# Optimization experiments

Hardware: AMD Instinct MI355X
Metric: run time of the kernel (lower is better)

Reference implementation:

```python
import jax, jax.numpy as jnp
import numpy as np

# dims
B, N, D = 256, 77, 768     # batch, CLIP tokens, token dim
K, Dn, H = 16, 768, 8      # nodes, node dim, heads
HID, L = 512, 2            # edge-MLP hidden, num GNN layers


def setup_inputs() -> dict:
    key = jax.random.key(0)
    ks = jax.random.split(key, 12)
    g = lambda k, shape, s=0.02: (jax.random.normal(k, shape, jnp.float32) * s)
    return {
        "w": jax.random.normal(ks[0], (B, N, D), jnp.float32),
        "token_mask": jax.random.randint(ks[1], (B, N), 0, 2).astype(jnp.int32),
        "node_queries": g(ks[2], (1, K, Dn)),
        "Wq": g(ks[3], (Dn, Dn)), "bq": jnp.zeros((Dn,), jnp.float32),
        "Wk": g(ks[4], (D, Dn)),  "bk": jnp.zeros((Dn,), jnp.float32),
        "Wv": g(ks[5], (D, Dn)),  "bv": jnp.zeros((Dn,), jnp.float32),
        "We1": g(ks[6], (2 * Dn, HID)), "be1": jnp.zeros((HID,), jnp.float32),
        "We2": g(ks[7], (HID, 1)),      "be2": jnp.zeros((1,), jnp.float32),
        "fuse_gate": jnp.float32(0.0),
        "Wg": g(ks[8], (L, Dn, Dn)), "bg": jnp.zeros((L, Dn), jnp.float32),
    }


def _edge_logits(V, We1, be1, We2, be2):
    # edge_mlp(cat[Vi, Vj]) without materializing [B,K,K,2Dn]:
    # split first linear into the Vi-half and Vj-half of its weight.
    hi = V @ We1[:Dn]   # [B,K,HID]
    hj = V @ We1[Dn:]   # [B,K,HID]
    h = jax.nn.relu(hi[:, :, None, :] + hj[:, None, :, :] + be1)  # [B,K,K,HID]
    return jnp.einsum('bijh,h->bij', h, We2[:, 0]) + be2[0]       # [B,K,K]


def _forward(w, node_queries, Wq, bq, Wk, bk, Wv, bv,
             We1, be1, We2, be2, fuse_gate, Wg, bg, token_mask):
    q = jnp.broadcast_to(node_queries, (B, K, Dn))
    Q = q @ Wq + bq        # [B,K,Dn]
    Kt = w @ Wk + bk       # [B,N,Dn]
    Vt = w @ Wv + bv       # [B,N,Dn]
    # per-head dot products summed over heads == full Dn dot product
    scale = (Dn // H) ** -0.5
    scores = jnp.einsum('bkd,bnd->bkn', Q, Kt) * scale  # [B,K,N]
    pad = (token_mask == 0)[:, None, :]                 # [B,1,N]
    scores = jnp.where(pad, jnp.finfo(scores.dtype).min, scores)
    # softmax over K per token (transpose to [B,N,K])
    S = jax.nn.softmax(jnp.swapaxes(scores, 1, 2), axis=-1)  # [B,N,K]
    V = jnp.einsum('bnk,bnd->bkd', S, Vt)                    # [B,K,Dn]
    gate = jax.nn.sigmoid(fuse_gate)
    V = (1.0 - gate) * V + gate * q
    # pre-GNN edge logits, then relational GNN refinement
    E = _edge_logits(V, We1, be1, We2, be2)
    A = jax.nn.softmax(E, axis=-1)  # [B,K,K], fixed across layers
    for l in range(L):
        msg = jnp.einsum('bij,bjd->bid', A, V @ Wg[l] + bg[l])
        V = V + jax.nn.relu(msg)
    # post-GNN edge logits
    E = _edge_logits(V, We1, be1, We2, be2)
    return S, V, E


def reference(w, token_mask, node_queries, Wq, bq, Wk, bk, Wv, bv,
              We1, be1, We2, be2, fuse_gate, Wg, bg):
    return _forward(w, node_queries, Wq, bq, Wk, bk, Wv, bv,
                    We1, be1, We2, be2, fuse_gate, Wg, bg, token_mask)
```

## Files before the change

kernel.cpp:

```cpp
#include <hip/hip_runtime.h>

typedef unsigned short u16;
typedef __attribute__((ext_vector_type(8))) short short8;
typedef __attribute__((ext_vector_type(4))) float f32x4;

#define DEV static __device__ __forceinline__

DEV float bf2f(u16 u) { return __uint_as_float(((unsigned)u) << 16); }
DEV u16 f2bf(float f) {
  unsigned u = __float_as_uint(f);
  return (u16)((u + 0x7fffu + ((u >> 16) & 1u)) >> 16);
}

DEV void cp16(void* lds, const void* g) {
  __builtin_amdgcn_global_load_lds(
      (const __attribute__((address_space(1))) unsigned int*)g,
      (__attribute__((address_space(3))) unsigned int*)lds, 16, 0, 0);
}

DEV void vm_drain() { asm volatile("s_waitcnt vmcnt(0)" ::: "memory"); }


__global__ __launch_bounds__(256) void tcast_all(const float* __restrict__ Wv,
                                                 const float* __restrict__ We1,
                                                 const float* __restrict__ Wg,
                                                 u16* __restrict__ WvT,
                                                 u16* __restrict__ We1T,
                                                 u16* __restrict__ WgT) {
  __shared__ float tile[32][33];
  const float* src; u16* dst; int C;
  switch (blockIdx.z) {
    case 0: src = Wv;           dst = WvT;           C = 768; break;
    case 1: src = We1;          dst = We1T;          C = 512; break;
    case 2: src = We1 + 393216; dst = We1T + 393216; C = 512; break;
    case 3: src = Wg;           dst = WgT;           C = 768; break;
    default: src = Wg + 589824; dst = WgT + 589824;  C = 768; break;
  }
  int r0 = blockIdx.y * 32, c0 = blockIdx.x * 32;
  if (c0 >= C) return;
  int tr = threadIdx.x >> 5, tc = threadIdx.x & 31;
#pragma unroll
  for (int rr = 0; rr < 4; ++rr)
    tile[tr + rr * 8][tc] = src[(size_t)(r0 + tr + rr * 8) * C + c0 + tc];
  __syncthreads();
#pragma unroll
  for (int rr = 0; rr < 4; ++rr)
    dst[(size_t)(c0 + tr + rr * 8) * 768 + r0 + tc] = f2bf(tile[tc][tr + rr * 8]);
}

__global__ __launch_bounds__(256) void q_part(const float* __restrict__ nq,
                                              const float* __restrict__ Wq,
                                              float* __restrict__ Qpart) {
  int gid = blockIdx.x * 256 + threadIdx.x;
  int s = blockIdx.y;
  int k = gid / 768, d = gid % 768;
  const float* nr = nq + k * 768 + s * 96;
  const float* wp = Wq + (size_t)(s * 96) * 768 + d;
  float s0 = 0.f, s1 = 0.f, s2 = 0.f, s3 = 0.f;
#pragma unroll
  for (int c = 0; c < 96; c += 4) {
    s0 += nr[c + 0] * wp[(size_t)(c + 0) * 768];
    s1 += nr[c + 1] * wp[(size_t)(c + 1) * 768];
    s2 += nr[c + 2] * wp[(size_t)(c + 2) * 768];
    s3 += nr[c + 3] * wp[(size_t)(c + 3) * 768];
  }
  Qpart[(size_t)s * 12288 + gid] = (s0 + s1) + (s2 + s3);
}

__global__ __launch_bounds__(256) void q_reduce(const float* __restrict__ Qpart,
                                                const float* __restrict__ bq,
                                                float* __restrict__ Qf) {
  int gid = blockIdx.x * 256 + threadIdx.x;
  int d = gid % 768;
  float s = bq[d];
#pragma unroll
  for (int i = 0; i < 8; ++i) s += Qpart[(size_t)i * 12288 + gid];
  Qf[gid] = s;
}

__global__ __launch_bounds__(256) void pt_kernel(const float* __restrict__ Qf,
                                                 const float* __restrict__ Wk,
                                                 const float* __restrict__ bk,
                                                 u16* __restrict__ PT16,
                                                 float* __restrict__ qb) {
  int t = threadIdx.x;
  if (blockIdx.x == 48) {
    int k = t >> 4, j = t & 15;
    const float* q = Qf + k * 768 + j * 48;
    const float* bp = bk + j * 48;
    float s = 0.f;
#pragma unroll
    for (int d = 0; d < 48; d += 4) {
      f32x4 qv = *(const f32x4*)&q[d];
      f32x4 bv4 = *(const f32x4*)&bp[d];
      s += qv[0] * bv4[0] + qv[1] * bv4[1] + qv[2] * bv4[2] + qv[3] * bv4[3];
    }
#pragma unroll
    for (int off = 1; off < 16; off <<= 1) s += __shfl_xor(s, off);
    if (j == 0) qb[k] = s;
    return;
  }
  int gid = blockIdx.x * 256 + t;
  int c = gid >> 4, k = gid & 15;
  const float* wr = Wk + (size_t)c * 768;
  const float* q = Qf + k * 768;
  float s = 0.f;
  for (int d = 0; d < 768; d += 4) {
    f32x4 wv = *(const f32x4*)&wr[d];
    f32x4 qv = *(const f32x4*)&q[d];
    s += wv[0] * qv[0] + wv[1] * qv[1] + wv[2] * qv[2] + wv[3] * qv[3];
  }
  PT16[k * 768 + c] = f2bf(s);
}

__global__ __launch_bounds__(256) void score2(const float* __restrict__ w,
                                              const u16* __restrict__ PT16,
                                              const float* __restrict__ qb,
                                              const int* __restrict__ mask,
                                              float* __restrict__ Sout) {
  __shared__ u16 Ps[16 * 776];
  int t = threadIdx.x, wave = t >> 6, lane = t & 63, l16 = lane & 15, quad = lane >> 4;
  int m0 = blockIdx.x * 64;
#pragma unroll
  for (int r = 0; r < 6; ++r) {
    int idx = t + 256 * r;
    int row = idx / 96, c8 = idx % 96;
    *(short8*)&Ps[row * 776 + c8 * 8] = *(const short8*)&PT16[row * 768 + c8 * 8];
  }
  __syncthreads();
  int row = m0 + wave * 16 + l16;
  const float* ap = w + (size_t)row * 768 + quad * 8;
  f32x4 acc = {0.f, 0.f, 0.f, 0.f};
#pragma unroll
  for (int it = 0; it < 24; ++it) {
    f32x4 a0 = *(const f32x4*)(ap + it * 32);
    f32x4 a1 = *(const f32x4*)(ap + it * 32 + 4);
    short8 fa;
#pragma unroll
    for (int e = 0; e < 4; ++e) { fa[e] = (short)f2bf(a0[e]); fa[e + 4] = (short)f2bf(a1[e]); }
    short8 fb = *(const short8*)&Ps[l16 * 776 + it * 32 + quad * 8];
    acc = __builtin_amdgcn_mfma_f32_16x16x32_bf16(fa, fb, acc, 0, 0, 0);
  }
  float qv = qb[l16];
  const float scale = 0.1020620726159658f;
#pragma unroll
  for (int r = 0; r < 4; ++r) {
    int orow = m0 + wave * 16 + quad * 4 + r;
    float s = (acc[r] + qv) * scale;
    if (mask[orow] == 0) s = -3.402823466e38f;
    float mx = s;
#pragma unroll
    for (int off = 1; off < 16; off <<= 1) mx = fmaxf(mx, __shfl_xor(mx, off));
    float e = __expf(s - mx);
    float sm = e;
#pragma unroll
    for (int off = 1; off < 16; off <<= 1) sm += __shfl_xor(sm, off);
    Sout[(size_t)orow * 16 + l16] = e / sm;
  }
}

__global__ __launch_bounds__(256) void u_kernel(const float* __restrict__ Sg,
                                                const float* __restrict__ w,
                                                u16* __restrict__ U16,
                                                float* __restrict__ sk) {
  __shared__ float Ss[1232];
  int b = blockIdx.x, t = threadIdx.x;
  int d = blockIdx.y * 256 + t;
#pragma unroll
  for (int r = 0; r < 5; ++r) {
    int idx = t + 256 * r;
    if (idx < 1232) Ss[idx] = Sg[(size_t)b * 1232 + idx];
  }
  __syncthreads();
  float a[16];
#pragma unroll
  for (int k = 0; k < 16; ++k) a[k] = 0.f;
  const float* wp = w + (size_t)b * 59136;
  for (int n = 0; n < 77; ++n) {
    float g = wp[(size_t)n * 768 + d];
    const float* sr = &Ss[n * 16];
#pragma unroll
    for (int k = 0; k < 16; ++k) a[k] += sr[k] * g;
  }
#pragma unroll
  for (int k = 0; k < 16; ++k)
    U16[(size_t)b * 12288 + (size_t)k * 768 + d] = f2bf(a[k]);
  if (blockIdx.y == 0 && t < 16) {
    float s = 0.f;
    for (int n = 0; n < 77; ++n) s += Ss[n * 16 + t];
    sk[b * 16 + t] = s;
  }
}

__global__ __launch_bounds__(256) void vgemm(const u16* __restrict__ A,
                                             const u16* __restrict__ BT,
                                             const float* __restrict__ skp,
                                             const float* __restrict__ bv,
                                             const float* __restrict__ nq,
                                             const float* __restrict__ gatep,
                                             float* __restrict__ V32,
                                             u16* __restrict__ V16) {
  __shared__ u16 As[2 * 64 * 32];
  __shared__ u16 Bs[2 * 128 * 32];
  int mi = blockIdx.x / 6, ni = blockIdx.x % 6;
  int m0 = mi * 64, n0 = ni * 128;
  int t = threadIdx.x;
  int wave = t >> 6, lane = t & 63, l16 = lane & 15, quad = lane >> 4;
  int ra = wave * 16 + (lane >> 2);
  int rb1 = wave * 32 + (lane >> 2);
  int rb2 = rb1 + 16;
  int cslot = lane & 3;
  int cga = (cslot ^ ((ra >> 1) & 3)) * 8;
  int cgb1 = (cslot ^ ((rb1 >> 1) & 3)) * 8;
  int cgb2 = (cslot ^ ((rb2 >> 1) & 3)) * 8;

  const u16* Ap = A + (size_t)(m0 + ra) * 768 + cga;
  const u16* Bp1 = BT + (size_t)(n0 + rb1) * 768 + cgb1;
  const u16* Bp2 = BT + (size_t)(n0 + rb2) * 768 + cgb2;
  u16* AsW = &As[(wave * 16) * 32];
  u16* BsW1 = &Bs[(wave * 32) * 32];
  u16* BsW2 = &Bs[(wave * 32 + 16) * 32];

  f32x4 zero4 = {0.f, 0.f, 0.f, 0.f};
  f32x4 acc[4][2];
#pragma unroll
  for (int i = 0; i < 4; ++i) { acc[i][0] = zero4; acc[i][1] = zero4; }

  cp16(AsW, Ap); cp16(BsW1, Bp1); cp16(BsW2, Bp2);
  vm_drain();
  __builtin_amdgcn_s_barrier();

  int cur = 0;
  for (int k0 = 0; k0 < 768; k0 += 32) {
    int nxt = cur ^ 1;
    if (k0 + 32 < 768) {
      cp16(AsW + nxt * 2048, Ap + k0 + 32);
      cp16(BsW1 + nxt * 4096, Bp1 + k0 + 32);
      cp16(BsW2 + nxt * 4096, Bp2 + k0 + 32);
    }
    const u16* Ab = &As[cur * 2048];
    const u16* Bb = &Bs[cur * 4096];
    short8 fa[4], fb[2];
#pragma unroll
    for (int i = 0; i < 4; ++i) {
      int R = i * 16 + l16;
      fa[i] = *(const short8*)&Ab[R * 32 + (quad ^ ((R >> 1) & 3)) * 8];
    }
#pragma unroll
    for (int j = 0; j < 2; ++j) {
      int R = wave * 32 + j * 16 + l16;
      fb[j] = *(const short8*)&Bb[R * 32 + (quad ^ ((R >> 1) & 3)) * 8];
    }
#pragma unroll
    for (int i = 0; i < 4; ++i)
#pragma unroll
      for (int j = 0; j < 2; ++j)
        acc[i][j] = __builtin_amdgcn_mfma_f32_16x16x32_bf16(fa[i], fb[j], acc[i][j], 0, 0, 0);
    vm_drain();
    __builtin_amdgcn_s_barrier();
    cur = nxt;
  }

  float gv = gatep[0];
  float g = 1.f / (1.f + __expf(-gv)), og = 1.f - g;
  int narr[2]; float bvj[2];
#pragma unroll
  for (int j = 0; j < 2; ++j) {
    narr[j] = n0 + wave * 32 + j * 16 + l16;
    bvj[j] = bv[narr[j]];
  }
#pragma unroll
  for (int i = 0; i < 4; ++i)
#pragma unroll
    for (int r = 0; r < 4; ++r) {
      int m = m0 + i * 16 + quad * 4 + r;
      float skv = skp[m];
      size_t mrow = (size_t)m * 768;
      const float* nqr = nq + (m & 15) * 768;
#pragma unroll
      for (int j = 0; j < 2; ++j) {
        float val = acc[i][j][r] + skv * bvj[j];
        float v = og * val + g * nqr[narr[j]];
        V32[mrow + narr[j]] = v;
        V16[mrow + narr[j]] = f2bf(v);
      }
    }
}

__global__ __launch_bounds__(256) void gemm16s(const u16* __restrict__ A,
                                               const u16* __restrict__ BT0,
                                               const float* __restrict__ bias0,
                                               u16* __restrict__ C0, int N0, int ntA,
                                               const u16* __restrict__ BT1,
                                               const float* __restrict__ bias1,
                                               u16* __restrict__ C1, int N1, int ntB,
                                               int K) {
  __shared__ u16 As[2 * 64 * 32];
  __shared__ u16 Bs[2 * 128 * 32];
  int nt = ntA + ntB;
  int mi = blockIdx.x / nt, ni = blockIdx.x % nt;
  const u16* BT; const float* bias; u16* C; int N, n0;
  if (ni < ntA) { BT = BT0; bias = bias0; C = C0; N = N0; n0 = ni * 128; }
  else          { BT = BT1; bias = bias1; C = C1; N = N1; n0 = (ni - ntA) * 128; }
  int m0 = mi * 64;
  int t = threadIdx.x;
  int wave = t >> 6, lane = t & 63, l16 = lane & 15, quad = lane >> 4;
  int ra = wave * 16 + (lane >> 2);
  int rb1 = wave * 32 + (lane >> 2);
  int rb2 = rb1 + 16;
  int cslot = lane & 3;
  int cga = (cslot ^ ((ra >> 1) & 3)) * 8;
  int cgb1 = (cslot ^ ((rb1 >> 1) & 3)) * 8;
  int cgb2 = (cslot ^ ((rb2 >> 1) & 3)) * 8;

  const u16* Ap = A + (size_t)(m0 + ra) * K + cga;
  const u16* Bp1 = BT + (size_t)(n0 + rb1) * K + cgb1;
  const u16* Bp2 = BT + (size_t)(n0 + rb2) * K + cgb2;
  u16* AsW = &As[(wave * 16) * 32];
  u16* BsW1 = &Bs[(wave * 32) * 32];
  u16* BsW2 = &Bs[(wave * 32 + 16) * 32];

  f32x4 zero4 = {0.f, 0.f, 0.f, 0.f};
  f32x4 acc[4][2];
#pragma unroll
  for (int i = 0; i < 4; ++i) { acc[i][0] = zero4; acc[i][1] = zero4; }

  cp16(AsW, Ap); cp16(BsW1, Bp1); cp16(BsW2, Bp2);
  vm_drain();
  __builtin_amdgcn_s_barrier();

  int cur = 0;
  for (int k0 = 0; k0 < K; k0 += 32) {
    int nxt = cur ^ 1;
    if (k0 + 32 < K) {
      cp16(AsW + nxt * 2048, Ap + k0 + 32);
      cp16(BsW1 + nxt * 4096, Bp1 + k0 + 32);
      cp16(BsW2 + nxt * 4096, Bp2 + k0 + 32);
    }
    const u16* Ab = &As[cur * 2048];
    const u16* Bb = &Bs[cur * 4096];
    short8 fa[4], fb[2];
#pragma unroll
    for (int i = 0; i < 4; ++i) {
      int R = i * 16 + l16;
      fa[i] = *(const short8*)&Ab[R * 32 + (quad ^ ((R >> 1) & 3)) * 8];
    }
#pragma unroll
    for (int j = 0; j < 2; ++j) {
      int R = wave * 32 + j * 16 + l16;
      fb[j] = *(const short8*)&Bb[R * 32 + (quad ^ ((R >> 1) & 3)) * 8];
    }
#pragma unroll
    for (int i = 0; i < 4; ++i)
#pragma unroll
      for (int j = 0; j < 2; ++j)
        acc[i][j] = __builtin_amdgcn_mfma_f32_16x16x32_bf16(fa[i], fb[j], acc[i][j], 0, 0, 0);
    vm_drain();
    __builtin_amdgcn_s_barrier();
    cur = nxt;
  }

  int narr[2]; float bvj[2];
#pragma unroll
  for (int j = 0; j < 2; ++j) {
    narr[j] = n0 + wave * 32 + j * 16 + l16;
    bvj[j] = bias ? bias[narr[j]] : 0.f;
  }
#pragma unroll
  for (int i = 0; i < 4; ++i)
#pragma unroll
    for (int r = 0; r < 4; ++r) {
      size_t mrow = (size_t)(m0 + i * 16 + quad * 4 + r) * N;
#pragma unroll
      for (int j = 0; j < 2; ++j)
        C[mrow + narr[j]] = f2bf(acc[i][j][r] + bvj[j]);
    }
}

__global__ __launch_bounds__(256) void edge_kernel(const u16* __restrict__ HIJ,
                                                   const float* __restrict__ be1,
                                                   const float* __restrict__ We2,
                                                   const float* __restrict__ be2v,
                                                   float* __restrict__ Aout,
                                                   float* __restrict__ Eout) {
  __shared__ float hiS[16 * 260];
  __shared__ float hjS[16 * 260];
  __shared__ float be1s[512];
  __shared__ float w2s[512];
  int b = blockIdx.x, t = threadIdx.x;
  be1s[t] = be1[t]; be1s[t + 256] = be1[t + 256];
  w2s[t] = We2[t];  w2s[t + 256] = We2[t + 256];

  int i = t >> 4, jj = t & 15;
  float e = 0.f;
  for (int half = 0; half < 2; ++half) {
    __syncthreads();
#pragma unroll
    for (int r = 0; r < 2; ++r) {
      int idx = t + 256 * r;
      int row = idx >> 5, c8 = idx & 31;
      const u16* src = &HIJ[(size_t)(b * 16 + row) * 1024 + half * 256 + c8 * 8];
      short8 hv = *(const short8*)src;
      short8 jv = *(const short8*)(src + 512);
      f32x4 l0, l1, m0v, m1v;
#pragma unroll
      for (int ee = 0; ee < 4; ++ee) {
        l0[ee] = bf2f((u16)hv[ee]); l1[ee] = bf2f((u16)hv[ee + 4]);
        m0v[ee] = bf2f((u16)jv[ee]); m1v[ee] = bf2f((u16)jv[ee + 4]);
      }
      *(f32x4*)&hiS[row * 260 + c8 * 8] = l0;
      *(f32x4*)&hiS[row * 260 + c8 * 8 + 4] = l1;
      *(f32x4*)&hjS[row * 260 + c8 * 8] = m0v;
      *(f32x4*)&hjS[row * 260 + c8 * 8 + 4] = m1v;
    }
    __syncthreads();
    const float* hi = &hiS[i * 260];
    const float* hj = &hjS[jj * 260];
    const float* b1 = &be1s[half * 256];
    const float* w2 = &w2s[half * 256];
#pragma unroll 2
    for (int h4 = 0; h4 < 64; ++h4) {
      f32x4 hv = *(const f32x4*)&hi[h4 * 4];
      f32x4 jv = *(const f32x4*)&hj[h4 * 4];
      f32x4 bv = *(const f32x4*)&b1[h4 * 4];
      f32x4 wv = *(const f32x4*)&w2[h4 * 4];
#pragma unroll
      for (int ee = 0; ee < 4; ++ee)
        e += fmaxf(hv[ee] + jv[ee] + bv[ee], 0.f) * wv[ee];
    }
  }
  e += be2v[0];

  if (Aout) {
    float mx = e;
#pragma unroll
    for (int off = 1; off < 16; off <<= 1) mx = fmaxf(mx, __shfl_xor(mx, off));
    float ex = __expf(e - mx);
    float sm = ex;
#pragma unroll
    for (int off = 1; off < 16; off <<= 1) sm += __shfl_xor(sm, off);
    Aout[(size_t)b * 256 + t] = ex / sm;
  }
  if (Eout) Eout[(size_t)b * 256 + t] = e;
}

__global__ __launch_bounds__(256) void combine_kernel(const float* __restrict__ Aws,
                                                      const u16* __restrict__ G,
                                                      float* __restrict__ V32,
                                                      u16* __restrict__ V16,
                                                      float* __restrict__ Vout) {
  __shared__ float Gs[16 * 772];
  __shared__ float As[256];
  int b = blockIdx.x, t = threadIdx.x;
#pragma unroll
  for (int r = 0; r < 6; ++r) {
    int idx = t + 256 * r;
    int row = idx / 96, c8 = idx % 96;
    short8 gv8 = *(const short8*)&G[(size_t)(b * 16 + row) * 768 + c8 * 8];
    f32x4 l0, l1;
#pragma unroll
    for (int ee = 0; ee < 4; ++ee) { l0[ee] = bf2f((u16)gv8[ee]); l1[ee] = bf2f((u16)gv8[ee + 4]); }
    *(f32x4*)&Gs[row * 772 + c8 * 8] = l0;
    *(f32x4*)&Gs[row * 772 + c8 * 8 + 4] = l1;
  }
  As[t] = Aws[(size_t)b * 256 + t];
  __syncthreads();
#pragma unroll
  for (int m = 0; m < 3; ++m) {
    int d = t + m * 256;
    float gv[16];
#pragma unroll
    for (int j = 0; j < 16; ++j) gv[j] = Gs[j * 772 + d];
#pragma unroll
    for (int i = 0; i < 16; ++i) {
      float msg = 0.f;
#pragma unroll
      for (int j = 0; j < 16; ++j) msg += As[i * 16 + j] * gv[j];
      size_t idx = (size_t)b * 12288 + (size_t)i * 768 + d;
      float v = V32[idx] + fmaxf(msg, 0.f);
      V32[idx] = v;
      V16[idx] = f2bf(v);
      if (Vout) Vout[idx] = v;
    }
  }
}

extern "C" void kernel_launch(void* const* d_in, const int* in_sizes, int n_in,
                              void* d_out, int out_size, void* d_ws, size_t ws_size,
                              hipStream_t stream) {
  const float* w    = (const float*)d_in[0];
  const int*   mask = (const int*)d_in[1];
  const float* nq   = (const float*)d_in[2];
  const float* Wq   = (const float*)d_in[3];
  const float* bq   = (const float*)d_in[4];
  const float* Wk   = (const float*)d_in[5];
  const float* bk   = (const float*)d_in[6];
  const float* Wv   = (const float*)d_in[7];
  const float* bv   = (const float*)d_in[8];
  const float* We1  = (const float*)d_in[9];
  const float* be1  = (const float*)d_in[10];
  const float* We2  = (const float*)d_in[11];
  const float* be2  = (const float*)d_in[12];
  const float* gate = (const float*)d_in[13];
  const float* Wg   = (const float*)d_in[14];
  const float* bg   = (const float*)d_in[15];

  float* ws    = (float*)d_ws;
  float* V32   = ws;
  float* Aws   = V32 + 3145728;
  float* Qpart = Aws + 65536;
  float* Qf    = Qpart + 98304;
  float* qb    = Qf + 12288;
  float* sk    = qb + 16;
  u16* PT16    = (u16*)(sk + 4096);
  u16* WvT     = PT16 + 12288;
  u16* We1T    = WvT + 589824;
  u16* WgT     = We1T + 786432;
  u16* V16     = WgT + 1179648;
  u16* U16     = V16 + 3145728;
  u16* HIJ     = U16 + 3145728;
  u16* Gws     = HIJ + 4194304;

  float* out  = (float*)d_out;
  float* Sout = out;
  float* Vout = out + 315392;
  float* Eout = out + 315392 + 3145728;

  dim3 blk(256);

  tcast_all<<<dim3(24, 24, 5), blk, 0, stream>>>(Wv, We1, Wg, WvT, We1T, WgT);
  q_part<<<dim3(48, 8), blk, 0, stream>>>(nq, Wq, Qpart);
  q_reduce<<<48, blk, 0, stream>>>(Qpart, bq, Qf);
  pt_kernel<<<49, blk, 0, stream>>>(Qf, Wk, bk, PT16, qb);

  score2<<<308, blk, 0, stream>>>(w, PT16, qb, mask, Sout);

  u_kernel<<<dim3(256, 3), blk, 0, stream>>>(Sout, w, U16, sk);
  vgemm<<<384, blk, 0, stream>>>(U16, WvT, sk, bv, nq, gate, V32, V16);

  gemm16s<<<896, blk, 0, stream>>>(V16, We1T, nullptr, HIJ, 1024, 8,
                                   WgT, bg, Gws, 768, 6, 768);
  edge_kernel<<<256, blk, 0, stream>>>(HIJ, be1, We2, be2, Aws, (float*)nullptr);
  combine_kernel<<<256, blk, 0, stream>>>(Aws, Gws, V32, V16, (float*)nullptr);

  gemm16s<<<384, blk, 0, stream>>>(V16, WgT + 589824, bg + 768, Gws, 768, 6,
                                   WgT + 589824, bg + 768, Gws, 768, 0, 768);
  combine_kernel<<<256, blk, 0, stream>>>(Aws, Gws, V32, V16, Vout);

  gemm16s<<<512, blk, 0, stream>>>(V16, We1T, nullptr, HIJ, 1024, 8,
                                   We1T, nullptr, HIJ, 1024, 0, 768);
  edge_kernel<<<256, blk, 0, stream>>>(HIJ, be1, We2, be2, (float*)nullptr, Eout);
}
```

Measured before the change: 330.4 us.

## Fuse score+U and edge+combine kernels, relax GEMM pipeline waits

Merges the score/softmax kernel with the S·w reduction into one per-batch kernel, so S goes straight to shared memory and w is reread from cache rather than through a separate launch. Also fuses the first edge-logit kernel with the first GNN combine step, and changes the double-buffered GEMM loops to wait only on the older prefetch (vmcnt(3)) instead of draining all loads. This cuts two kernel launches and one global round-trip of S and A. In exchange, parallelism drops from 308+768 blocks to 256 blocks with heavier per-thread register use.

```diff
diff --git a/kernel.cpp b/kernel.cpp
--- a/kernel.cpp
+++ b/kernel.cpp
@@ -17,8 +17,6 @@
       (const __attribute__((address_space(1))) unsigned int*)g,
       (__attribute__((address_space(3))) unsigned int*)lds, 16, 0, 0);
 }
-
-DEV void vm_drain() { asm volatile("s_waitcnt vmcnt(0)" ::: "memory"); }
 
 
 __global__ __launch_bounds__(256) void tcast_all(const float* __restrict__ Wv,
@@ -113,14 +111,17 @@
   PT16[k * 768 + c] = f2bf(s);
 }
 
-__global__ __launch_bounds__(256) void score2(const float* __restrict__ w,
-                                              const u16* __restrict__ PT16,
-                                              const float* __restrict__ qb,
-                                              const int* __restrict__ mask,
-                                              float* __restrict__ Sout) {
+__global__ __launch_bounds__(256) void scoreu_kernel(const float* __restrict__ w,
+                                                     const u16* __restrict__ PT16,
+                                                     const float* __restrict__ qb,
+                                                     const int* __restrict__ mask,
+                                                     float* __restrict__ Sout,
+                                                     u16* __restrict__ U16,
+                                                     float* __restrict__ sk) {
   __shared__ u16 Ps[16 * 776];
-  int t = threadIdx.x, wave = t >> 6, lane = t & 63, l16 = lane & 15, quad = lane >> 4;
-  int m0 = blockIdx.x * 64;
+  __shared__ float Ss[80 * 16];
+  int b = blockIdx.x, t = threadIdx.x;
+  int wave = t >> 6, lane = t & 63, l16 = lane & 15, quad = lane >> 4;
 #pragma unroll
   for (int r = 0; r < 6; ++r) {
     int idx = t + 256 * r;
@@ -128,64 +129,65 @@
     *(short8*)&Ps[row * 776 + c8 * 8] = *(const short8*)&PT16[row * 768 + c8 * 8];
   }
   __syncthreads();
-  int row = m0 + wave * 16 + l16;
-  const float* ap = w + (size_t)row * 768 + quad * 8;
-  f32x4 acc = {0.f, 0.f, 0.f, 0.f};
-#pragma unroll
-  for (int it = 0; it < 24; ++it) {
-    f32x4 a0 = *(const f32x4*)(ap + it * 32);
-    f32x4 a1 = *(const f32x4*)(ap + it * 32 + 4);
-    short8 fa;
-#pragma unroll
-    for (int e = 0; e < 4; ++e) { fa[e] = (short)f2bf(a0[e]); fa[e + 4] = (short)f2bf(a1[e]); }
-    short8 fb = *(const short8*)&Ps[l16 * 776 + it * 32 + quad * 8];
-    acc = __builtin_amdgcn_mfma_f32_16x16x32_bf16(fa, fb, acc, 0, 0, 0);
-  }
+  const float scale = 0.1020620726159658f;
   float qv = qb[l16];
-  const float scale = 0.1020620726159658f;
-#pragma unroll
-  for (int r = 0; r < 4; ++r) {
-    int orow = m0 + wave * 16 + quad * 4 + r;
-    float s = (acc[r] + qv) * scale;
-    if (mask[orow] == 0) s = -3.402823466e38f;
-    float mx = s;
-#pragma unroll
-    for (int off = 1; off < 16; off <<= 1) mx = fmaxf(mx, __shfl_xor(mx, off));
-    float e = __expf(s - mx);
-    float sm = e;
-#pragma unroll
-    for (int off = 1; off < 16; off <<= 1) sm += __shfl_xor(sm, off);
-    Sout[(size_t)orow * 16 + l16] = e / sm;
-  }
-}
-
-__global__ __launch_bounds__(256) void u_kernel(const float* __restrict__ Sg,
-                                                const float* __restrict__ w,
-                                                u16* __restrict__ U16,
-                                                float* __restrict__ sk) {
-  __shared__ float Ss[1232];
-  int b = blockIdx.x, t = threadIdx.x;
-  int d = blockIdx.y * 256 + t;
-#pragma unroll
-  for (int r = 0; r < 5; ++r) {
-    int idx = t + 256 * r;
-    if (idx < 1232) Ss[idx] = Sg[(size_t)b * 1232 + idx];
+  for (int tile = wave; tile < 5; tile += 4) {
+    int nrow = tile * 16 + l16;
+    int nclamp = nrow < 77 ? nrow : 76;
+    const float* ap = w + ((size_t)b * 77 + nclamp) * 768 + quad * 8;
+    f32x4 acc = {0.f, 0.f, 0.f, 0.f};
+#pragma unroll
+    for (int it = 0; it < 24; ++it) {
+      f32x4 a0 = *(const f32x4*)(ap + it * 32);
+      f32x4 a1 = *(const f32x4*)(ap + it * 32 + 4);
+      short8 fa;
+#pragma unroll
+      for (int e = 0; e < 4; ++e) { fa[e] = (short)f2bf(a0[e]); fa[e + 4] = (short)f2bf(a1[e]); }
+      short8 fb = *(const short8*)&Ps[l16 * 776 + it * 32 + quad * 8];
+      acc = __builtin_amdgcn_mfma_f32_16x16x32_bf16(fa, fb, acc, 0, 0, 0);
+    }
+#pragma unroll
+    for (int r = 0; r < 4; ++r) {
+      int n_r = tile * 16 + quad * 4 + r;
+      if (n_r < 77) {
+        float s = (acc[r] + qv) * scale;
+        if (mask[b * 77 + n_r] == 0) s = -3.402823466e38f;
+        float mx = s;
+#pragma unroll
+        for (int off = 1; off < 16; off <<= 1) mx = fmaxf(mx, __shfl_xor(mx, off));
+        float e = __expf(s - mx);
+        float sm = e;
+#pragma unroll
+        for (int off = 1; off < 16; off <<= 1) sm += __shfl_xor(sm, off);
+        float p = e / sm;
+        Sout[((size_t)b * 77 + n_r) * 16 + l16] = p;
+        Ss[n_r * 16 + l16] = p;
+      }
+    }
   }
   __syncthreads();
-  float a[16];
-#pragma unroll
-  for (int k = 0; k < 16; ++k) a[k] = 0.f;
-  const float* wp = w + (size_t)b * 59136;
+  float a0[16], a1[16], a2[16];
+#pragma unroll
+  for (int k = 0; k < 16; ++k) { a0[k] = 0.f; a1[k] = 0.f; a2[k] = 0.f; }
+  const float* wb = w + (size_t)b * 59136;
   for (int n = 0; n < 77; ++n) {
-    float g = wp[(size_t)n * 768 + d];
+    const float* wr = wb + (size_t)n * 768;
+    float w0 = wr[t], w1 = wr[t + 256], w2 = wr[t + 512];
     const float* sr = &Ss[n * 16];
 #pragma unroll
-    for (int k = 0; k < 16; ++k) a[k] += sr[k] * g;
-  }
-#pragma unroll
-  for (int k = 0; k < 16; ++k)
-    U16[(size_t)b * 12288 + (size_t)k * 768 + d] = f2bf(a[k]);
-  if (blockIdx.y == 0 && t < 16) {
+    for (int k = 0; k < 16; ++k) {
+      float s = sr[k];
+      a0[k] += s * w0; a1[k] += s * w1; a2[k] += s * w2;
+    }
+  }
+  u16* ub = U16 + (size_t)b * 12288;
+#pragma unroll
+  for (int k = 0; k < 16; ++k) {
+    ub[k * 768 + t] = f2bf(a0[k]);
+    ub[k * 768 + t + 256] = f2bf(a1[k]);
+    ub[k * 768 + t + 512] = f2bf(a2[k]);
+  }
+  if (t < 16) {
     float s = 0.f;
     for (int n = 0; n < 77; ++n) s += Ss[n * 16 + t];
     sk[b * 16 + t] = s;
@@ -227,8 +229,6 @@
   for (int i = 0; i < 4; ++i) { acc[i][0] = zero4; acc[i][1] = zero4; }
 
   cp16(AsW, Ap); cp16(BsW1, Bp1); cp16(BsW2, Bp2);
-  vm_drain();
-  __builtin_amdgcn_s_barrier();
 
   int cur = 0;
   for (int k0 = 0; k0 < 768; k0 += 32) {
@@ -237,7 +237,11 @@
       cp16(AsW + nxt * 2048, Ap + k0 + 32);
       cp16(BsW1 + nxt * 4096, Bp1 + k0 + 32);
       cp16(BsW2 + nxt * 4096, Bp2 + k0 + 32);
-    }
+      asm volatile("s_waitcnt vmcnt(3)" ::: "memory");
+    } else {
+      asm volatile("s_waitcnt vmcnt(0)" ::: "memory");
+    }
+    asm volatile("s_barrier" ::: "memory");
     const u16* Ab = &As[cur * 2048];
     const u16* Bb = &Bs[cur * 4096];
     short8 fa[4], fb[2];
@@ -256,8 +260,7 @@
 #pragma unroll
       for (int j = 0; j < 2; ++j)
         acc[i][j] = __builtin_amdgcn_mfma_f32_16x16x32_bf16(fa[i], fb[j], acc[i][j], 0, 0, 0);
-    vm_drain();
-    __builtin_amdgcn_s_barrier();
+    asm volatile("s_barrier" ::: "memory");
     cur = nxt;
   }
 
@@ -326,8 +329,6 @@
   for (int i = 0; i < 4; ++i) { acc[i][0] = zero4; acc[i][1] = zero4; }
 
   cp16(AsW, Ap); cp16(BsW1, Bp1); cp16(BsW2, Bp2);
-  vm_drain();
-  __builtin_amdgcn_s_barrier();
 
   int cur = 0;
   for (int k0 = 0; k0 < K; k0 += 32) {
@@ -336,7 +337,11 @@
       cp16(AsW + nxt * 2048, Ap + k0 + 32);
       cp16(BsW1 + nxt * 4096, Bp1 + k0 + 32);
       cp16(BsW2 + nxt * 4096, Bp2 + k0 + 32);
-    }
+      asm volatile("s_waitcnt vmcnt(3)" ::: "memory");
+    } else {
+      asm volatile("s_waitcnt vmcnt(0)" ::: "memory");
+    }
+    asm volatile("s_barrier" ::: "memory");
     const u16* Ab = &As[cur * 2048];
     const u16* Bb = &Bs[cur * 4096];
     short8 fa[4], fb[2];
@@ -355,8 +360,7 @@
 #pragma unroll
       for (int j = 0; j < 2; ++j)
         acc[i][j] = __builtin_amdgcn_mfma_f32_16x16x32_bf16(fa[i], fb[j], acc[i][j], 0, 0, 0);
-    vm_drain();
-    __builtin_amdgcn_s_barrier();
+    asm volatile("s_barrier" ::: "memory");
     cur = nxt;
   }
 
@@ -442,6 +446,108 @@
     Aout[(size_t)b * 256 + t] = ex / sm;
   }
   if (Eout) Eout[(size_t)b * 256 + t] = e;
+}
+
+__global__ __launch_bounds__(256) void edgecombine_kernel(const u16* __restrict__ HIJ,
+                                                          const float* __restrict__ be1,
+                                                          const float* __restrict__ We2,
+                                                          const float* __restrict__ be2v,
+                                                          float* __restrict__ Aout,
+                                                          const u16* __restrict__ G,
+                                                          float* __restrict__ V32,
+                                                          u16* __restrict__ V16) {
+  __shared__ float buf[16 * 772];
+  __shared__ float be1s[512];
+  __shared__ float w2s[512];
+  __shared__ float As_s[256];
+  float* hiS = buf;
+  float* hjS = buf + 16 * 260;
+  int b = blockIdx.x, t = threadIdx.x;
+  be1s[t] = be1[t]; be1s[t + 256] = be1[t + 256];
+  w2s[t] = We2[t];  w2s[t + 256] = We2[t + 256];
+
+  int i = t >> 4, jj = t & 15;
+  float e = 0.f;
+  for (int half = 0; half < 2; ++half) {
+    __syncthreads();
+#pragma unroll
+    for (int r = 0; r < 2; ++r) {
+      int idx = t + 256 * r;
+      int row = idx >> 5, c8 = idx & 31;
+      const u16* src = &HIJ[(size_t)(b * 16 + row) * 1024 + half * 256 + c8 * 8];
+      short8 hv = *(const short8*)src;
+      short8 jv = *(const short8*)(src + 512);
+      f32x4 l0, l1, m0v, m1v;
+#pragma unroll
+      for (int ee = 0; ee < 4; ++ee) {
+        l0[ee] = bf2f((u16)hv[ee]); l1[ee] = bf2f((u16)hv[ee + 4]);
+        m0v[ee] = bf2f((u16)jv[ee]); m1v[ee] = bf2f((u16)jv[ee + 4]);
+      }
+      *(f32x4*)&hiS[row * 260 + c8 * 8] = l0;
+      *(f32x4*)&hiS[row * 260 + c8 * 8 + 4] = l1;
+      *(f32x4*)&hjS[row * 260 + c8 * 8] = m0v;
+      *(f32x4*)&hjS[row * 260 + c8 * 8 + 4] = m1v;
+    }
+    __syncthreads();
+    const float* hi = &hiS[i * 260];
+    const float* hj = &hjS[jj * 260];
+    const float* b1 = &be1s[half * 256];
+    const float* w2 = &w2s[half * 256];
+#pragma unroll 2
+    for (int h4 = 0; h4 < 64; ++h4) {
+      f32x4 hv = *(const f32x4*)&hi[h4 * 4];
+      f32x4 jv = *(const f32x4*)&hj[h4 * 4];
+      f32x4 bv = *(const f32x4*)&b1[h4 * 4];
+      f32x4 wv = *(const f32x4*)&w2[h4 * 4];
+#pragma unroll
+      for (int ee = 0; ee < 4; ++ee)
+        e += fmaxf(hv[ee] + jv[ee] + bv[ee], 0.f) * wv[ee];
+    }
+  }
+  e += be2v[0];
+
+  float mx = e;
+#pragma unroll
+  for (int off = 1; off < 16; off <<= 1) mx = fmaxf(mx, __shfl_xor(mx, off));
+  float ex = __expf(e - mx);
+  float sm = ex;
+#pragma unroll
+  for (int off = 1; off < 16; off <<= 1) sm += __shfl_xor(sm, off);
+  float p = ex / sm;
+  As_s[t] = p;
+  Aout[(size_t)b * 256 + t] = p;
+  __syncthreads();
+
+  float* Gs = buf;
+#pragma unroll
+  for (int r = 0; r < 6; ++r) {
+    int idx = t + 256 * r;
+    int row = idx / 96, c8 = idx % 96;
+    short8 gv8 = *(const short8*)&G[(size_t)(b * 16 + row) * 768 + c8 * 8];
+    f32x4 l0, l1;
+#pragma unroll
+    for (int ee = 0; ee < 4; ++ee) { l0[ee] = bf2f((u16)gv8[ee]); l1[ee] = bf2f((u16)gv8[ee + 4]); }
+    *(f32x4*)&Gs[row * 772 + c8 * 8] = l0;
+    *(f32x4*)&Gs[row * 772 + c8 * 8 + 4] = l1;
+  }
+  __syncthreads();
+#pragma unroll
+  for (int m = 0; m < 3; ++m) {
+    int d = t + m * 256;
+    float gv[16];
+#pragma unroll
+    for (int j = 0; j < 16; ++j) gv[j] = Gs[j * 772 + d];
+#pragma unroll
+    for (int ii = 0; ii < 16; ++ii) {
+      float msg = 0.f;
+#pragma unroll
+      for (int j = 0; j < 16; ++j) msg += As_s[ii * 16 + j] * gv[j];
+      size_t idx = (size_t)b * 12288 + (size_t)ii * 768 + d;
+      float v = V32[idx] + fmaxf(msg, 0.f);
+      V32[idx] = v;
+      V16[idx] = f2bf(v);
+    }
+  }
 }
 
 __global__ __launch_bounds__(256) void combine_kernel(const float* __restrict__ Aws,
@@ -533,15 +639,13 @@
   q_reduce<<<48, blk, 0, stream>>>(Qpart, bq, Qf);
   pt_kernel<<<49, blk, 0, stream>>>(Qf, Wk, bk, PT16, qb);
 
-  score2<<<308, blk, 0, stream>>>(w, PT16, qb, mask, Sout);
-
-  u_kernel<<<dim3(256, 3), blk, 0, stream>>>(Sout, w, U16, sk);
+  scoreu_kernel<<<256, blk, 0, stream>>>(w, PT16, qb, mask, Sout, U16, sk);
+
   vgemm<<<384, blk, 0, stream>>>(U16, WvT, sk, bv, nq, gate, V32, V16);
 
   gemm16s<<<896, blk, 0, stream>>>(V16, We1T, nullptr, HIJ, 1024, 8,
                                    WgT, bg, Gws, 768, 6, 768);
-  edge_kernel<<<256, blk, 0, stream>>>(HIJ, be1, We2, be2, Aws, (float*)nullptr);
-  combine_kernel<<<256, blk, 0, stream>>>(Aws, Gws, V32, V16, (float*)nullptr);
+  edgecombine_kernel<<<256, blk, 0, stream>>>(HIJ, be1, We2, be2, Aws, Gws, V32, V16);
 
   gemm16s<<<384, blk, 0, stream>>>(V16, WgT + 589824, bg + 768, Gws, 768, 6,
                                    WgT + 589824, bg + 768, Gws, 768, 0, 768);
```

After: 363.3 us. +10.0%, slower.
